# Performance work log

Hardware: AMD Instinct MI355X
Metric: run time of the kernel (lower is better)

Reference implementation:

```python
import jax, jax.numpy as jnp
import numpy as np

DM = 1024        # model dim
E = 32           # totalexperts = expertsets*nexperts = 8*4
FE = 128         # expertsize
T = 4            # sparsity = nexperts (tokens per group)
EPS_TIEBREAK = 1e-6


def setup_inputs() -> dict:
    key = jax.random.key(0)
    k0, k1, k2, k3 = jax.random.split(key, 4)
    x = jax.random.normal(k0, (4, 4096, DM), dtype=jnp.float32)
    # fan_in-style inits matching misc.get_init_weight / get_init_bias
    controller = jax.random.normal(k1, (DM, E), dtype=jnp.float32) / np.float32(np.sqrt(DM))
    f1 = jax.random.normal(k2, (DM, E, FE), dtype=jnp.float32) / np.float32(np.sqrt(DM))
    bias = jnp.zeros((E, FE), dtype=jnp.float32)
    f2 = jax.random.normal(k3, (E, FE, DM), dtype=jnp.float32) / np.float32(np.sqrt(E * FE / T))
    return {"x": x, "controller": controller, "f1": f1, "bias": bias, "f2": f2}


def reference(x, controller, f1, bias, f2):
    B, S, d = x.shape
    t = T
    g = S // t
    # '... (b t) d -> ... b t d'
    grouped = x.reshape(B, g, t, d)
    # controller logits: '... t d, d e -> ... t e'
    logits = jnp.einsum('bgtd,de->bgte', grouped, controller)
    # deterministic tie-break offset over the t (slot) axis
    logits = logits + jnp.linspace(0.0, EPS_TIEBREAK, t, dtype=logits.dtype)[:, None]
    # softmax over dim=1 (group axis) as in original
    probs = jax.nn.softmax(logits, axis=1)
    # hard argmax mask over dim=-3 (group axis), scaled by soft probs
    perm = (logits == jnp.max(logits, axis=1, keepdims=True)).astype(x.dtype) * probs
    # expert up-projection with soft permutation: '... t d, d e f, ... t e -> ... e f'
    inner = jnp.einsum('bgtd,def,bgte->bgef', grouped, f1, perm)
    inner = jax.nn.relu(inner + bias)
    # expert down-projection: '... e f, e f d -> ... e d'
    inter = jnp.einsum('bgef,efd->bged', inner, f2)
    # unpermute: '... e d, ... t e -> ... t d'
    res = jnp.einsum('bged,bgte->bgtd', inter, perm)
    return res.reshape(B, S, d)
```

## Files before the change

kernel.cpp:

```cpp
#include <hip/hip_runtime.h>
#include <math.h>


#define DM   1024
#define NE   32
#define FE   128
#define T4   4
#define SS   4096
#define NGRP 1024
#define NROW 512
#define LP_STRIDE (NROW * NGRP)
#define VP_OFF   524288

__global__ __launch_bounds__(256, 3)
void k_logits(const float* __restrict__ x, const float* __restrict__ ctrl,
              float* __restrict__ Lp, float* __restrict__ out)
{
    const int m      = blockIdx.x;
    const int ks     = blockIdx.y;
    const int tid    = threadIdx.x;
    const int base_s = m * 128;
    const int b      = base_s >> 12;
    const int g0     = (base_s & 4095) >> 2;

    __shared__ float xT[2][32 * 132];
    __shared__ float cs[2][32 * 32];

    const int tq = tid & 31;
    const int eg = tid >> 5;

    float acc[4][4];
#pragma unroll
    for (int i = 0; i < 4; ++i)
#pragma unroll
        for (int j = 0; j < 4; ++j) acc[i][j] = 0.f;

    const int srow = tid >> 1;
    const int sq   = tid & 1;

    float4 px[4];
    float4 pc;

    const float* xrow = x + (size_t)(base_s + srow) * DM + sq * 16;

    {
        const int k0 = ks * 256;
#pragma unroll
        for (int cr = 0; cr < 4; ++cr) px[cr] = *(const float4*)(xrow + k0 + cr * 4);
        pc = ((const float4*)(ctrl + (size_t)k0 * NE))[tid];
#pragma unroll
        for (int cr = 0; cr < 4; ++cr) {
            const int d = (sq * 4 + cr) * 4;
            const float4 v = px[cr];
            xT[0][(d + 0) * 132 + srow] = v.x;
            xT[0][(d + 1) * 132 + srow] = v.y;
            xT[0][(d + 2) * 132 + srow] = v.z;
            xT[0][(d + 3) * 132 + srow] = v.w;
        }
        ((float4*)cs[0])[tid] = pc;
    }
    __syncthreads();

    for (int kit = 0; kit < 8; ++kit) {
        if (kit < 7) {
            const int k0 = ks * 256 + (kit + 1) * 32;
#pragma unroll
            for (int cr = 0; cr < 4; ++cr) px[cr] = *(const float4*)(xrow + k0 + cr * 4);
            pc = ((const float4*)(ctrl + (size_t)k0 * NE))[tid];
        }

        const float* xb = xT[kit & 1];
        const float* cb = cs[kit & 1];
#pragma unroll 8
        for (int d = 0; d < 32; ++d) {
            const float4 xv = *(const float4*)(xb + d * 132 + tq * 4);
            const float4 cv = *(const float4*)(cb + d * 32 + eg * 4);
            const float xa[4] = { xv.x, xv.y, xv.z, xv.w };
            const float ca[4] = { cv.x, cv.y, cv.z, cv.w };
#pragma unroll
            for (int i = 0; i < 4; ++i)
#pragma unroll
                for (int j = 0; j < 4; ++j) acc[i][j] += xa[i] * ca[j];
        }

        if (kit < 7) {
            const int nb = (kit + 1) & 1;
#pragma unroll
            for (int cr = 0; cr < 4; ++cr) {
                const int d = (sq * 4 + cr) * 4;
                const float4 v = px[cr];
                xT[nb][(d + 0) * 132 + srow] = v.x;
                xT[nb][(d + 1) * 132 + srow] = v.y;
                xT[nb][(d + 2) * 132 + srow] = v.z;
                xT[nb][(d + 3) * 132 + srow] = v.w;
            }
            ((float4*)cs[nb])[tid] = pc;
        }
        __syncthreads();
    }

    {
        float* Lb = Lp + (size_t)ks * LP_STRIDE;
        const int g = g0 + tq;
#pragma unroll
        for (int i = 0; i < 4; ++i)
#pragma unroll
            for (int j = 0; j < 4; ++j) {
                const int row = (b * T4 + i) * NE + eg * 4 + j;
                Lb[(size_t)row * NGRP + g] = acc[i][j];
            }
    }

    {
        const float4 z = make_float4(0.f, 0.f, 0.f, 0.f);
        float4* o4 = (float4*)(out + (size_t)(base_s + ks * 32) * DM);
#pragma unroll 4
        for (int i = tid; i < 32 * DM / 4; i += 256) o4[i] = z;
    }
}

__global__ __launch_bounds__(256)
void k_route(float* __restrict__ Lp)
{
    __shared__ float rmx[4], rs[4];
    __shared__ int   rgm[4];

    const int r   = blockIdx.x;
    const int tid = threadIdx.x;
    const float* L0 = Lp + (size_t)r * NGRP;

    const int g0c = tid * 4;
    const float4 v0 = *(const float4*)(L0 + g0c);
    const float4 v1 = *(const float4*)(L0 + 1 * LP_STRIDE + g0c);
    const float4 v2 = *(const float4*)(L0 + 2 * LP_STRIDE + g0c);
    const float4 v3 = *(const float4*)(L0 + 3 * LP_STRIDE + g0c);
    const float l[4] = { v0.x + v1.x + v2.x + v3.x,
                         v0.y + v1.y + v2.y + v3.y,
                         v0.z + v1.z + v2.z + v3.z,
                         v0.w + v1.w + v2.w + v3.w };
    float mx = -INFINITY, s = 0.f;
    int gm = 0;
#pragma unroll
    for (int j = 0; j < 4; ++j) {
        const float lv = l[j];
        if (lv > mx) { s = s * __expf(mx - lv) + 1.f; mx = lv; gm = g0c + j; }
        else         { s += __expf(lv - mx); }
    }
#pragma unroll
    for (int off = 1; off < 64; off <<= 1) {
        const float m2 = __shfl_xor(mx, off);
        const float s2 = __shfl_xor(s, off);
        const int   g2 = __shfl_xor(gm, off);
        const float mn = fmaxf(mx, m2);
        s  = s * __expf(mx - mn) + s2 * __expf(m2 - mn);
        gm = (m2 > mx) ? g2 : ((m2 == mx && g2 < gm) ? g2 : gm);
        mx = mn;
    }
    if ((tid & 63) == 0) {
        const int w = tid >> 6;
        rmx[w] = mx; rs[w] = s; rgm[w] = gm;
    }
    __syncthreads();
    if (tid == 0) {
        float M = rmx[0], S = rs[0];
        int   G = rgm[0];
#pragma unroll
        for (int wv = 1; wv < 4; ++wv) {
            const float m2 = rmx[wv], s2 = rs[wv];
            const int   g2 = rgm[wv];
            const float mn = fmaxf(M, m2);
            S = S * __expf(M - mn) + s2 * __expf(m2 - mn);
            G = (m2 > M) ? g2 : ((m2 == M && g2 < G) ? g2 : G);
            M = mn;
        }
        ((int*)Lp)[(size_t)r * NGRP] = G;
        Lp[(size_t)r * NGRP + 1] = 1.f / S;
    }
}

__global__ __launch_bounds__(256, 2)
void k_up(const float* __restrict__ x, const float* __restrict__ f1,
          float* __restrict__ ws)
{
    const int e   = blockIdx.x & 31;
    const int dc  = blockIdx.x >> 5;
    const int tid = threadIdx.x;

    __shared__ float xs[16 * 68];
    __shared__ int   gS[16];

    if (tid < 16) {
        const int r = tid * NE + e;
        gS[tid] = ((const int*)ws)[(size_t)r * NGRP];
    }
    __syncthreads();

    {
        const int row = tid >> 4;
        const int f4c = tid & 15;
        const int bq = row >> 2, t = row & 3;
        const int s = bq * SS + gS[row] * 4 + t;
        const float4 v = *(const float4*)(x + (size_t)s * DM + dc * 64 + f4c * 4);
        xs[row * 68 + f4c * 4 + 0] = v.x;
        xs[row * 68 + f4c * 4 + 1] = v.y;
        xs[row * 68 + f4c * 4 + 2] = v.z;
        xs[row * 68 + f4c * 4 + 3] = v.w;
    }
    __syncthreads();

    const int f4 = tid & 31;
    const int rw = tid >> 5;
    const float* f1p = f1 + (size_t)(dc * 64) * (NE * FE) + e * FE + f4 * 4;
    const float* x0 = xs + rw * 68;
    const float* x1 = xs + (rw + 8) * 68;

    float a0[4] = {0.f, 0.f, 0.f, 0.f}, a1[4] = {0.f, 0.f, 0.f, 0.f};
#pragma unroll 16
    for (int dl = 0; dl < 64; ++dl) {
        const float4 w4 = *(const float4*)(f1p + (size_t)dl * (NE * FE));
        const float xa = x0[dl], xb = x1[dl];
        a0[0] += xa * w4.x; a0[1] += xa * w4.y; a0[2] += xa * w4.z; a0[3] += xa * w4.w;
        a1[0] += xb * w4.x; a1[1] += xb * w4.y; a1[2] += xb * w4.z; a1[3] += xb * w4.w;
    }

    float* Vp = ws + VP_OFF + (size_t)(dc * 32 + e) * (16 * FE);
    *(float4*)(Vp + rw       * FE + f4 * 4) = make_float4(a0[0], a0[1], a0[2], a0[3]);
    *(float4*)(Vp + (rw + 8) * FE + f4 * 4) = make_float4(a1[0], a1[1], a1[2], a1[3]);
}

__global__ __launch_bounds__(256, 2)
void k_down(const float* __restrict__ f2, const float* __restrict__ bias,
            const float* __restrict__ ws, float* __restrict__ out)
{
    const int e   = blockIdx.x & 31;
    const int dt  = (blockIdx.x >> 5) & 7;
    const int rh  = blockIdx.x >> 8;
    const int tid = threadIdx.x;

    __shared__ float vv[8 * 132];
    __shared__ float hs[8 * 132];
    __shared__ int   gS[8];
    __shared__ float pS[8];

    if (tid < 8) {
        const int r = (rh * 8 + tid) * NE + e;
        gS[tid] = ((const int*)ws)[(size_t)r * NGRP];
        pS[tid] = ws[(size_t)r * NGRP + 1];
    }

    {
        const float* Vp = ws + VP_OFF;
        const int row = tid >> 5, f4 = tid & 31;
        float4 s = make_float4(0.f, 0.f, 0.f, 0.f);
#pragma unroll
        for (int dc = 0; dc < 16; ++dc) {
            const float4 v = *(const float4*)(Vp + (size_t)(dc * 32 + e) * (16 * FE)
                                                 + (rh * 8 + row) * FE + f4 * 4);
            s.x += v.x; s.y += v.y; s.z += v.z; s.w += v.w;
        }
        *(float4*)(vv + row * 132 + f4 * 4) = s;
    }
    __syncthreads();

    {
#pragma unroll
        for (int q = 0; q < 4; ++q) {
            const int idx = tid + q * 256;
            const int row = idx >> 7, f = idx & 127;
            const int qb = row & ~3;
            float u = bias[e * FE + f];
#pragma unroll
            for (int t2 = 0; t2 < T4; ++t2)
                if (gS[qb + t2] == gS[row]) u += pS[qb + t2] * vv[(qb + t2) * 132 + f];
            hs[row * 132 + f] = pS[row] * fmaxf(u, 0.f);
        }
    }
    __syncthreads();

    const int d4 = tid & 31;
    const int rw = tid >> 5;
    const float* f2p = f2 + (size_t)e * FE * DM + dt * 128 + d4 * 4;
    const float* hp  = hs + rw * 132;

    float a[4] = {0.f, 0.f, 0.f, 0.f};
#pragma unroll 16
    for (int f = 0; f < FE; ++f) {
        const float4 w4 = *(const float4*)(f2p + (size_t)f * DM);
        const float ha = hp[f];
        a[0] += ha * w4.x; a[1] += ha * w4.y; a[2] += ha * w4.z; a[3] += ha * w4.w;
    }

    const int grow = rh * 8 + rw;
    const int bq = grow >> 2, t = grow & 3;
    float* orow = out + ((size_t)(bq * SS + gS[rw] * 4 + t)) * DM + dt * 128 + d4 * 4;
    atomicAdd(orow + 0, a[0]);
    atomicAdd(orow + 1, a[1]);
    atomicAdd(orow + 2, a[2]);
    atomicAdd(orow + 3, a[3]);
}

extern "C" void kernel_launch(void* const* d_in, const int* in_sizes, int n_in,
                              void* d_out, int out_size, void* d_ws, size_t ws_size,
                              hipStream_t stream)
{
    const float* x    = (const float*)d_in[0];
    const float* ctrl = (const float*)d_in[1];
    const float* f1   = (const float*)d_in[2];
    const float* bias = (const float*)d_in[3];
    const float* f2   = (const float*)d_in[4];
    float* out = (float*)d_out;
    float* ws  = (float*)d_ws;

    k_logits<<<dim3(128, 4), 256, 0, stream>>>(x, ctrl, ws, out);
    k_route <<<dim3(512),    256, 0, stream>>>(ws);
    k_up    <<<dim3(512),    256, 0, stream>>>(x, f1, ws);
    k_down  <<<dim3(512),    256, 0, stream>>>(f2, bias, ws, out);
}
```

Before: 189.9 us.

## Split output zeroing into its own kernel and halve logits block tile

Moves zeroing of the output buffer out of the logits GEMM into a separate k_zero kernel. The logits kernel now uses 128-thread blocks covering 64 rows instead of 128, which doubles the grid to 1024 blocks for better CU coverage. The cost is an extra kernel launch and smaller per-block tiles, which means more redundant loads of the controller weights.

```diff
diff --git a/kernel.cpp b/kernel.cpp
--- a/kernel.cpp
+++ b/kernel.cpp
@@ -12,22 +12,31 @@
 #define LP_STRIDE (NROW * NGRP)
 #define VP_OFF   524288
 
-__global__ __launch_bounds__(256, 3)
+__global__ __launch_bounds__(256)
+void k_zero(float* __restrict__ out)
+{
+    const float4 z = make_float4(0.f, 0.f, 0.f, 0.f);
+    float4* o4 = (float4*)out + (size_t)blockIdx.x * 2048;
+#pragma unroll
+    for (int j = 0; j < 8; ++j) o4[j * 256 + threadIdx.x] = z;
+}
+
+__global__ __launch_bounds__(128, 3)
 void k_logits(const float* __restrict__ x, const float* __restrict__ ctrl,
-              float* __restrict__ Lp, float* __restrict__ out)
+              float* __restrict__ Lp)
 {
     const int m      = blockIdx.x;
     const int ks     = blockIdx.y;
     const int tid    = threadIdx.x;
-    const int base_s = m * 128;
+    const int base_s = m * 64;
     const int b      = base_s >> 12;
     const int g0     = (base_s & 4095) >> 2;
 
-    __shared__ float xT[2][32 * 132];
+    __shared__ float xT[2][32 * 68];
     __shared__ float cs[2][32 * 32];
 
-    const int tq = tid & 31;
-    const int eg = tid >> 5;
+    const int tq = tid & 15;
+    const int eg = tid >> 4;
 
     float acc[4][4];
 #pragma unroll
@@ -37,43 +46,45 @@
 
     const int srow = tid >> 1;
     const int sq   = tid & 1;
+    const float* xrow = x + (size_t)(base_s + srow) * DM + ks * 256 + sq * 16;
 
     float4 px[4];
-    float4 pc;
-
-    const float* xrow = x + (size_t)(base_s + srow) * DM + sq * 16;
-
-    {
-        const int k0 = ks * 256;
-#pragma unroll
-        for (int cr = 0; cr < 4; ++cr) px[cr] = *(const float4*)(xrow + k0 + cr * 4);
-        pc = ((const float4*)(ctrl + (size_t)k0 * NE))[tid];
+    float4 pc[2];
+
+    {
+#pragma unroll
+        for (int cr = 0; cr < 4; ++cr) px[cr] = *(const float4*)(xrow + cr * 4);
+        const float4* cg = (const float4*)(ctrl + (size_t)(ks * 256) * NE);
+        pc[0] = cg[tid]; pc[1] = cg[tid + 128];
 #pragma unroll
         for (int cr = 0; cr < 4; ++cr) {
             const int d = (sq * 4 + cr) * 4;
             const float4 v = px[cr];
-            xT[0][(d + 0) * 132 + srow] = v.x;
-            xT[0][(d + 1) * 132 + srow] = v.y;
-            xT[0][(d + 2) * 132 + srow] = v.z;
-            xT[0][(d + 3) * 132 + srow] = v.w;
-        }
-        ((float4*)cs[0])[tid] = pc;
+            xT[0][(d + 0) * 68 + srow] = v.x;
+            xT[0][(d + 1) * 68 + srow] = v.y;
+            xT[0][(d + 2) * 68 + srow] = v.z;
+            xT[0][(d + 3) * 68 + srow] = v.w;
+        }
+        ((float4*)cs[0])[tid]       = pc[0];
+        ((float4*)cs[0])[tid + 128] = pc[1];
     }
     __syncthreads();
 
     for (int kit = 0; kit < 8; ++kit) {
         if (kit < 7) {
-            const int k0 = ks * 256 + (kit + 1) * 32;
-#pragma unroll
-            for (int cr = 0; cr < 4; ++cr) px[cr] = *(const float4*)(xrow + k0 + cr * 4);
-            pc = ((const float4*)(ctrl + (size_t)k0 * NE))[tid];
+            const int koff = (kit + 1) * 32;
+#pragma unroll
+            for (int cr = 0; cr < 4; ++cr)
+                px[cr] = *(const float4*)(xrow + koff + cr * 4);
+            const float4* cg = (const float4*)(ctrl + (size_t)(ks * 256 + koff) * NE);
+            pc[0] = cg[tid]; pc[1] = cg[tid + 128];
         }
 
         const float* xb = xT[kit & 1];
         const float* cb = cs[kit & 1];
 #pragma unroll 8
         for (int d = 0; d < 32; ++d) {
-            const float4 xv = *(const float4*)(xb + d * 132 + tq * 4);
+            const float4 xv = *(const float4*)(xb + d * 68 + tq * 4);
             const float4 cv = *(const float4*)(cb + d * 32 + eg * 4);
             const float xa[4] = { xv.x, xv.y, xv.z, xv.w };
             const float ca[4] = { cv.x, cv.y, cv.z, cv.w };
@@ -89,12 +100,13 @@
             for (int cr = 0; cr < 4; ++cr) {
                 const int d = (sq * 4 + cr) * 4;
                 const float4 v = px[cr];
-                xT[nb][(d + 0) * 132 + srow] = v.x;
-                xT[nb][(d + 1) * 132 + srow] = v.y;
-                xT[nb][(d + 2) * 132 + srow] = v.z;
-                xT[nb][(d + 3) * 132 + srow] = v.w;
+                xT[nb][(d + 0) * 68 + srow] = v.x;
+                xT[nb][(d + 1) * 68 + srow] = v.y;
+                xT[nb][(d + 2) * 68 + srow] = v.z;
+                xT[nb][(d + 3) * 68 + srow] = v.w;
             }
-            ((float4*)cs[nb])[tid] = pc;
+            ((float4*)cs[nb])[tid]       = pc[0];
+            ((float4*)cs[nb])[tid + 128] = pc[1];
         }
         __syncthreads();
     }
@@ -109,13 +121,6 @@
                 const int row = (b * T4 + i) * NE + eg * 4 + j;
                 Lb[(size_t)row * NGRP + g] = acc[i][j];
             }
-    }
-
-    {
-        const float4 z = make_float4(0.f, 0.f, 0.f, 0.f);
-        float4* o4 = (float4*)(out + (size_t)(base_s + ks * 32) * DM);
-#pragma unroll 4
-        for (int i = tid; i < 32 * DM / 4; i += 256) o4[i] = z;
     }
 }
 
@@ -311,7 +316,8 @@
     float* out = (float*)d_out;
     float* ws  = (float*)d_ws;
 
-    k_logits<<<dim3(128, 4), 256, 0, stream>>>(x, ctrl, ws, out);
+    k_zero  <<<dim3(2048),   256, 0, stream>>>(out);
+    k_logits<<<dim3(256, 4), 128, 0, stream>>>(x, ctrl, ws);
     k_route <<<dim3(512),    256, 0, stream>>>(ws);
     k_up    <<<dim3(512),    256, 0, stream>>>(x, f1, ws);
     k_down  <<<dim3(512),    256, 0, stream>>>(f2, bias, ws, out);
```

After: 191.5 us. About the same (+0.8%).
